# Kernel optimization log

Measured on AMD Instinct MI355X. Metric: run time of the kernel, lower is better.

The kernel has to match this reference:

```python
import jax, jax.numpy as jnp
import numpy as np

B, A, D, F, O, NB = 64, 1024, 5, 256, 256, 6  # batch, max_atoms, max_degree, ishape, oshape, bond feat dim


def setup_inputs() -> dict:
    key = jax.random.key(0)
    k1, k2, k3, k4 = jax.random.split(key, 4)
    atoms = jax.random.normal(k1, (B, A, F), dtype=jnp.float32)
    bonds = jax.random.normal(k2, (B, A, D, NB), dtype=jnp.float32)
    # -1 marks missing neighbor (degree padding); valid indices in [0, A)
    edges = jax.random.randint(k3, (B, A, D), -1, A)
    # xavier-normal-ish init for the 6 degree-specific weights, stacked [6, F+NB, O]
    scale = (2.0 / (F + NB + O)) ** 0.5
    degW = jax.random.normal(k4, (6, F + NB, O), dtype=jnp.float32) * scale
    b = jnp.full((1, O), 0.01, dtype=jnp.float32)
    return {"atoms": atoms, "bonds": bonds, "edges": edges, "degW": degW, "b": b}


def reference(atoms, bonds, edges, degW, b):
    # atoms: [B, A, F]; bonds: [B, A, D, NB]; edges: [B, A, D] int (-1 = pad)
    degrees = (edges != -1).sum(-1, keepdims=True)  # [B, A, 1]
    # pad a zero row at index 0 so edge -1 -> 0 gathers the mask value 0
    padded = jnp.pad(atoms, ((0, 0), (1, 0), (0, 0)))  # [B, A+1, F]
    neigh = jax.vmap(lambda p, e: p[e])(padded, edges + 1)  # [B, A, D, F]
    summed_atom = atoms + neigh.sum(axis=2)  # include_self=True
    feats = jnp.concatenate([summed_atom, bonds.sum(axis=2)], axis=-1)  # [B, A, F+NB]
    out = jnp.zeros((atoms.shape[0], atoms.shape[1], degW.shape[-1]), atoms.dtype)
    for d in range(6):  # fixed small structural loop over degree buckets
        mask = (degrees == d).astype(atoms.dtype)  # [B, A, 1]
        out = out + jax.nn.sigmoid(feats @ degW[d] + b) * mask
    return out
```

## Files before the change

### kernel.cpp

```cpp
#include <hip/hip_runtime.h>
#include <cstdint>

#define BATCH  64
#define NATOMS 1024
#define DEG    5
#define FIN    256
#define OOUT   256
#define NBF    6
#define KDIM   262
#define KP     288
#define MROWS  (BATCH * NATOMS)

typedef __attribute__((ext_vector_type(8))) short bf16x8;
typedef __attribute__((ext_vector_type(4))) float f32x4;

__device__ __forceinline__ unsigned short f2bf(float x) {
    unsigned u = __float_as_uint(x);
    u += 0x7fff + ((u >> 16) & 1);
    return (unsigned short)(u >> 16);
}
__device__ __forceinline__ float bf2f(unsigned short h) {
    return __uint_as_float(((unsigned)h) << 16);
}
__device__ __forceinline__ float sigmoidf_(float x) {
    return 1.f / (1.f + __expf(-x));
}

__global__ __launch_bounds__(256)
void convert_w_kernel(const float* __restrict__ degW, unsigned short* __restrict__ Wt)
{
    const int idx = blockIdx.x * 256 + threadIdx.x;
    if (idx >= 6 * KP * OOUT) return;
    const int d   = idx / (KP * OOUT);
    const int rem = idx % (KP * OOUT);
    const int k   = rem / OOUT;
    const int o   = rem % OOUT;
    const float v = (k < KDIM) ? degW[(size_t)d * KDIM * OOUT + (size_t)k * OOUT + o] : 0.f;
    Wt[(size_t)d * OOUT * KP + (size_t)o * KP + k] = f2bf(v);
}

__global__ __launch_bounds__(256)
void gather_kernel(const float* __restrict__ atoms, const float* __restrict__ bonds,
                   const int* __restrict__ edges, unsigned short* __restrict__ feats,
                   int* __restrict__ odd_list, int* __restrict__ odd_cnt)
{
    const int tid  = threadIdx.x;
    const int lane = tid & 63;
    const int w    = tid >> 6;
    const int row  = blockIdx.x * 4 + w;
    const int batch = row >> 10;

    const float4* arow = (const float4*)(atoms + (size_t)row * FIN);
    float4 v = arow[lane];
    int deg = 0;
    #pragma unroll
    for (int d = 0; d < DEG; ++d) {
        const int e = edges[row * DEG + d];
        if (e >= 0) {
            ++deg;
            const float4* nrow = (const float4*)(atoms + ((size_t)(batch << 10) + e) * FIN);
            const float4 nv = nrow[lane];
            v.x += nv.x; v.y += nv.y; v.z += nv.z; v.w += nv.w;
        }
    }
    ushort4 us;
    us.x = f2bf(v.x); us.y = f2bf(v.y); us.z = f2bf(v.z); us.w = f2bf(v.w);
    *(ushort4*)&feats[(size_t)row * KP + lane * 4] = us;

    if (lane < 32) {
        float bv = 0.f;
        if (lane < NBF) {
            const float* bb = bonds + (size_t)row * (DEG * NBF);
            #pragma unroll
            for (int d = 0; d < DEG; ++d) bv += bb[d * NBF + lane];
        }
        feats[(size_t)row * KP + FIN + lane] = f2bf(bv);
    }
    if (lane == 0 && deg != DEG) {
        const int i = atomicAdd(odd_cnt, 1);
        odd_list[i] = (row << 3) | deg;
    }
}

__global__ __launch_bounds__(256, 2)
void gemm_kernel(const unsigned short* __restrict__ feats,
                 const unsigned short* __restrict__ Wt5,
                 const float* __restrict__ bias, float* __restrict__ out)
{
    __shared__ short As[128 * 40];
    __shared__ short Bs[128 * 40];

    const int tid  = threadIdx.x;
    const int m0   = (blockIdx.x >> 1) * 128;
    const int n0   = (blockIdx.x & 1) * 128;
    const int lane = tid & 63;
    const int wave = tid >> 6;
    const int wm   = (wave & 1) * 64;
    const int wn   = (wave >> 1) * 64;
    const int fr   = lane & 15;
    const int q    = lane >> 4;

    f32x4 acc[4][4];
    #pragma unroll
    for (int i = 0; i < 4; ++i)
        #pragma unroll
        for (int j = 0; j < 4; ++j)
            acc[i][j] = (f32x4){0.f, 0.f, 0.f, 0.f};

    const unsigned short* Ag = feats + (size_t)m0 * KP;
    const unsigned short* Bg = Wt5  + (size_t)n0 * KP;

    for (int kt = 0; kt < KP; kt += 32) {
        __syncthreads();
        #pragma unroll
        for (int p = 0; p < 2; ++p) {
            const int idx = p * 256 + tid;
            const int r = idx >> 2, c = (idx & 3) * 8;
            *(uint4*)&As[r * 40 + c] = *(const uint4*)&Ag[(size_t)r * KP + kt + c];
            *(uint4*)&Bs[r * 40 + c] = *(const uint4*)&Bg[(size_t)r * KP + kt + c];
        }
        __syncthreads();

        bf16x8 af[4], bf[4];
        #pragma unroll
        for (int i = 0; i < 4; ++i)
            af[i] = *(const bf16x8*)&As[(wm + i * 16 + fr) * 40 + q * 8];
        #pragma unroll
        for (int j = 0; j < 4; ++j)
            bf[j] = *(const bf16x8*)&Bs[(wn + j * 16 + fr) * 40 + q * 8];
        #pragma unroll
        for (int i = 0; i < 4; ++i)
            #pragma unroll
            for (int j = 0; j < 4; ++j)
                acc[i][j] = __builtin_amdgcn_mfma_f32_16x16x32_bf16(af[i], bf[j], acc[i][j], 0, 0, 0);
    }

    #pragma unroll
    for (int j = 0; j < 4; ++j) {
        const int gn = n0 + wn + j * 16 + fr;
        const float bj = bias[gn];
        #pragma unroll
        for (int i = 0; i < 4; ++i) {
            #pragma unroll
            for (int r = 0; r < 4; ++r) {
                const int gm = m0 + wm + i * 16 + q * 4 + r;
                out[(size_t)gm * OOUT + gn] = sigmoidf_(acc[i][j][r] + bj);
            }
        }
    }
}

__global__ __launch_bounds__(256)
void fixup_kernel(const unsigned short* __restrict__ feats, const float* __restrict__ degW,
                  const float* __restrict__ bias, const int* __restrict__ odd_list,
                  const int* __restrict__ odd_cnt, float* __restrict__ out)
{
    const int cnt = *odd_cnt;
    const int tid = threadIdx.x;
    for (int i = blockIdx.x; i < cnt; i += gridDim.x) {
        const int packed = odd_list[i];
        const int row = packed >> 3;
        const int d   = packed & 7;
        const float* __restrict__ W = degW + (size_t)d * KDIM * OOUT;
        float acc = 0.f;
        for (int k = 0; k < KDIM; ++k)
            acc += bf2f(feats[(size_t)row * KP + k]) * W[(size_t)k * OOUT + tid];
        out[(size_t)row * OOUT + tid] = sigmoidf_(acc + bias[tid]);
    }
}

#define MT  32
#define KT  32
#define KPAD 288
__global__ __launch_bounds__(256, 2)
void nfp_conv_fallback(const float* __restrict__ atoms, const float* __restrict__ bonds,
                       const int* __restrict__ edges, const float* __restrict__ degW,
                       const float* __restrict__ bias, float* __restrict__ out)
{
    __shared__ float feats[MT * KPAD];
    __shared__ float wtile[KT * OOUT];
    __shared__ int   edg[MT * DEG];
    __shared__ int   deg_lds[MT];
    __shared__ int   odd_list[MT];
    __shared__ int   odd_cnt;
    __shared__ float b_lds[OOUT];

    const int tid = threadIdx.x, bid = blockIdx.x;
    const int batch = bid >> 5, a0 = (bid & 31) * MT;
    const size_t atom_base = (size_t)batch * NATOMS;

    b_lds[tid] = bias[tid];
    if (tid == 0) odd_cnt = 0;
    if (tid < MT * DEG) {
        const int m = tid / DEG, d = tid % DEG;
        edg[tid] = edges[(atom_base + a0 + m) * DEG + d];
    }
    __syncthreads();
    if (tid < MT) {
        int dc = 0;
        #pragma unroll
        for (int d = 0; d < DEG; ++d) dc += (edg[tid * DEG + d] != -1) ? 1 : 0;
        deg_lds[tid] = dc;
        if (dc != DEG) { const int idx = atomicAdd(&odd_cnt, 1); odd_list[idx] = tid; }
    }
    __syncthreads();
    {
        const int f = tid;
        for (int m = 0; m < MT; ++m) {
            float v = atoms[(atom_base + a0 + m) * FIN + f];
            #pragma unroll
            for (int d = 0; d < DEG; ++d) {
                const int e = edg[m * DEG + d];
                if (e >= 0) v += atoms[(atom_base + e) * FIN + f];
            }
            feats[m * KPAD + f] = v;
        }
        #pragma unroll
        for (int t = 0; t < 4; ++t) {
            const int idx = t * 256 + tid;
            const int m = idx >> 5, kk = idx & 31;
            float v = 0.f;
            if (kk < NBF) {
                const size_t bb = (atom_base + a0 + m) * (size_t)(DEG * NBF);
                #pragma unroll
                for (int d = 0; d < DEG; ++d) v += bonds[bb + d * NBF + kk];
            }
            feats[m * KPAD + FIN + kk] = v;
        }
    }
    const float* __restrict__ W5 = degW + (size_t)DEG * KDIM * OOUT;
    float acc[4][8];
    #pragma unroll
    for (int i = 0; i < 4; ++i)
        #pragma unroll
        for (int j = 0; j < 8; ++j) acc[i][j] = 0.f;
    const int tx = tid & 31, ty = tid >> 5;
    for (int kt = 0; kt < KPAD; kt += KT) {
        __syncthreads();
        #pragma unroll
        for (int t = 0; t < KT; ++t) {
            const int k = kt + t;
            wtile[t * OOUT + tid] = (k < KDIM) ? W5[(size_t)k * OOUT + tid] : 0.f;
        }
        __syncthreads();
        #pragma unroll 4
        for (int r = 0; r < KT; ++r) {
            float a_frag[4];
            #pragma unroll
            for (int i = 0; i < 4; ++i) a_frag[i] = feats[(ty * 4 + i) * KPAD + kt + r];
            float w_frag[8];
            #pragma unroll
            for (int j = 0; j < 8; ++j) w_frag[j] = wtile[r * OOUT + tx + j * 32];
            #pragma unroll
            for (int i = 0; i < 4; ++i)
                #pragma unroll
                for (int j = 0; j < 8; ++j) acc[i][j] += a_frag[i] * w_frag[j];
        }
    }
    #pragma unroll
    for (int i = 0; i < 4; ++i) {
        const int m = ty * 4 + i;
        if (deg_lds[m] == DEG) {
            const size_t row = (atom_base + a0 + m) * (size_t)OOUT;
            #pragma unroll
            for (int j = 0; j < 8; ++j) {
                const int o = tx + j * 32;
                out[row + o] = sigmoidf_(acc[i][j] + b_lds[o]);
            }
        }
    }
    const int ocnt = odd_cnt;
    for (int i = 0; i < ocnt; ++i) {
        const int m = odd_list[i], d = deg_lds[m];
        const float* __restrict__ W = degW + (size_t)d * KDIM * OOUT;
        float a2 = 0.f;
        for (int k = 0; k < KDIM; ++k) a2 += feats[m * KPAD + k] * W[(size_t)k * OOUT + tid];
        const size_t row = (atom_base + a0 + m) * (size_t)OOUT;
        out[row + tid] = sigmoidf_(a2 + b_lds[tid]);
    }
}

extern "C" void kernel_launch(void* const* d_in, const int* in_sizes, int n_in,
                              void* d_out, int out_size, void* d_ws, size_t ws_size,
                              hipStream_t stream) {
    const float* atoms = (const float*)d_in[0];
    const float* bonds = (const float*)d_in[1];
    const int*   edges = (const int*)d_in[2];
    const float* degW  = (const float*)d_in[3];
    const float* bias  = (const float*)d_in[4];
    float* out = (float*)d_out;

    const size_t FEATS_BYTES = (size_t)MROWS * KP * 2;
    const size_t WT_OFF      = FEATS_BYTES;
    const size_t WT_BYTES    = (size_t)6 * OOUT * KP * 2;
    const size_t ODD_OFF     = WT_OFF + WT_BYTES;
    const size_t ODD_BYTES   = (size_t)MROWS * 4;
    const size_t CNT_OFF     = ODD_OFF + ODD_BYTES;
    const size_t NEEDED      = CNT_OFF + 16;

    if (ws_size < NEEDED) {
        nfp_conv_fallback<<<BATCH * (NATOMS / MT), 256, 0, stream>>>(
            atoms, bonds, edges, degW, bias, out);
        return;
    }

    unsigned short* feats = (unsigned short*)d_ws;
    unsigned short* Wt    = (unsigned short*)((char*)d_ws + WT_OFF);
    int* odd_list         = (int*)((char*)d_ws + ODD_OFF);
    int* odd_cnt          = (int*)((char*)d_ws + CNT_OFF);

    hipMemsetAsync(odd_cnt, 0, 4, stream);
    convert_w_kernel<<<(6 * KP * OOUT) / 256, 256, 0, stream>>>(degW, Wt);
    gather_kernel<<<MROWS / 4, 256, 0, stream>>>(atoms, bonds, edges, feats, odd_list, odd_cnt);
    gemm_kernel<<<(MROWS / 128) * 2, 256, 0, stream>>>(
        feats, Wt + (size_t)5 * OOUT * KP, bias, out);
    fixup_kernel<<<512, 256, 0, stream>>>(feats, degW, bias, odd_list, odd_cnt, out);
}
```

Measured before the change: 222.1 us.

## Fuse gather, GEMM and odd-degree fixup into one kernel with pre-swizzled weights

Merges the neighbour gather, the degree-5 MFMA GEMM and the odd-degree fixup into one kernel. Each block builds a 64-row bf16 feature tile in LDS and reads weight fragments straight from global memory in a layout pre-swizzled to match MFMA operands. This removes the global feats round trip, the memset, the atomic odd list and two launches. Blocks are also mapped so each XCD handles whole batches, for L2 locality on neighbour gathers. The cost is that odd-degree rows are handled serially per block with scalar FMA loops, and weights are no longer staged in LDS.

```diff
diff --git a/kernel.cpp b/kernel.cpp
--- a/kernel.cpp
+++ b/kernel.cpp
@@ -9,7 +9,10 @@
 #define NBF    6
 #define KDIM   262
 #define KP     288
+#define NKT    9
 #define MROWS  (BATCH * NATOMS)
+#define MT     64
+#define AS     296
 
 typedef __attribute__((ext_vector_type(8))) short bf16x8;
 typedef __attribute__((ext_vector_type(4))) float f32x4;
@@ -27,78 +30,84 @@
 }
 
 __global__ __launch_bounds__(256)
-void convert_w_kernel(const float* __restrict__ degW, unsigned short* __restrict__ Wt)
+void convert_w_kernel(const float* __restrict__ degW, unsigned short* __restrict__ Wsw)
 {
     const int idx = blockIdx.x * 256 + threadIdx.x;
-    if (idx >= 6 * KP * OOUT) return;
-    const int d   = idx / (KP * OOUT);
-    const int rem = idx % (KP * OOUT);
-    const int k   = rem / OOUT;
-    const int o   = rem % OOUT;
-    const float v = (k < KDIM) ? degW[(size_t)d * KDIM * OOUT + (size_t)k * OOUT + o] : 0.f;
-    Wt[(size_t)d * OOUT * KP + (size_t)o * KP + k] = f2bf(v);
-}
-
-__global__ __launch_bounds__(256)
-void gather_kernel(const float* __restrict__ atoms, const float* __restrict__ bonds,
-                   const int* __restrict__ edges, unsigned short* __restrict__ feats,
-                   int* __restrict__ odd_list, int* __restrict__ odd_cnt)
+    if (idx >= 16 * NKT * 64) return;
+    const int lane = idx & 63;
+    const int t    = (idx >> 6) % NKT;
+    const int g    = (idx >> 6) / NKT;
+    const int col  = g * 16 + (lane & 15);
+    const int k0   = t * 32 + (lane >> 4) * 8;
+    const float* __restrict__ W5 = degW + (size_t)DEG * KDIM * OOUT;
+    unsigned short* dst = Wsw + (size_t)idx * 8;
+    #pragma unroll
+    for (int j = 0; j < 8; ++j) {
+        const int k = k0 + j;
+        dst[j] = f2bf((k < KDIM) ? W5[(size_t)k * OOUT + col] : 0.f);
+    }
+}
+
+__global__ __launch_bounds__(256, 4)
+void nfp_fused_kernel(const float* __restrict__ atoms, const float* __restrict__ bonds,
+                      const int* __restrict__ edges, const unsigned short* __restrict__ Wsw,
+                      const float* __restrict__ degW, const float* __restrict__ bias,
+                      float* __restrict__ out)
 {
+    __shared__ short Afeat[MT * AS];
+    __shared__ int   edg[MT * DEG];
+    __shared__ int   deg_lds[MT];
+
     const int tid  = threadIdx.x;
     const int lane = tid & 63;
-    const int w    = tid >> 6;
-    const int row  = blockIdx.x * 4 + w;
-    const int batch = row >> 10;
-
-    const float4* arow = (const float4*)(atoms + (size_t)row * FIN);
-    float4 v = arow[lane];
-    int deg = 0;
-    #pragma unroll
-    for (int d = 0; d < DEG; ++d) {
-        const int e = edges[row * DEG + d];
-        if (e >= 0) {
-            ++deg;
-            const float4* nrow = (const float4*)(atoms + ((size_t)(batch << 10) + e) * FIN);
-            const float4 nv = nrow[lane];
-            v.x += nv.x; v.y += nv.y; v.z += nv.z; v.w += nv.w;
-        }
-    }
-    ushort4 us;
-    us.x = f2bf(v.x); us.y = f2bf(v.y); us.z = f2bf(v.z); us.w = f2bf(v.w);
-    *(ushort4*)&feats[(size_t)row * KP + lane * 4] = us;
-
-    if (lane < 32) {
-        float bv = 0.f;
-        if (lane < NBF) {
-            const float* bb = bonds + (size_t)row * (DEG * NBF);
-            #pragma unroll
-            for (int d = 0; d < DEG; ++d) bv += bb[d * NBF + lane];
-        }
-        feats[(size_t)row * KP + FIN + lane] = f2bf(bv);
-    }
-    if (lane == 0 && deg != DEG) {
-        const int i = atomicAdd(odd_cnt, 1);
-        odd_list[i] = (row << 3) | deg;
-    }
-}
-
-__global__ __launch_bounds__(256, 2)
-void gemm_kernel(const unsigned short* __restrict__ feats,
-                 const unsigned short* __restrict__ Wt5,
-                 const float* __restrict__ bias, float* __restrict__ out)
-{
-    __shared__ short As[128 * 40];
-    __shared__ short Bs[128 * 40];
-
-    const int tid  = threadIdx.x;
-    const int m0   = (blockIdx.x >> 1) * 128;
-    const int n0   = (blockIdx.x & 1) * 128;
-    const int lane = tid & 63;
     const int wave = tid >> 6;
-    const int wm   = (wave & 1) * 64;
-    const int wn   = (wave >> 1) * 64;
-    const int fr   = lane & 15;
-    const int q    = lane >> 4;
+
+    const int bid   = blockIdx.x;
+    const int xcd   = bid & 7;
+    const int per   = bid >> 3;
+    const int batch = (per >> 4) * 8 + xcd;
+    const int blk   = per & 15;
+    const int row0  = batch * NATOMS + blk * MT;
+
+    for (int i = tid; i < MT * DEG; i += 256)
+        edg[i] = edges[row0 * DEG + i];
+    __syncthreads();
+    if (tid < MT) {
+        int dc = 0;
+        #pragma unroll
+        for (int d = 0; d < DEG; ++d) dc += (edg[tid * DEG + d] != -1) ? 1 : 0;
+        deg_lds[tid] = dc;
+    }
+
+    for (int mi = 0; mi < 16; ++mi) {
+        const int m = wave * 16 + mi;
+        float4 v = *(const float4*)&atoms[((size_t)row0 + m) * FIN + lane * 4];
+        #pragma unroll
+        for (int d = 0; d < DEG; ++d) {
+            const int e = edg[m * DEG + d];
+            if (e >= 0) {
+                const float4 nv = *(const float4*)&atoms[((size_t)(batch << 10) + e) * FIN + lane * 4];
+                v.x += nv.x; v.y += nv.y; v.z += nv.z; v.w += nv.w;
+            }
+        }
+        ushort4 us;
+        us.x = f2bf(v.x); us.y = f2bf(v.y); us.z = f2bf(v.z); us.w = f2bf(v.w);
+        *(ushort4*)&Afeat[m * AS + lane * 4] = us;
+        if (lane < 32) {
+            float bv = 0.f;
+            if (lane < NBF) {
+                const float* bb = bonds + ((size_t)row0 + m) * (DEG * NBF);
+                #pragma unroll
+                for (int d = 0; d < DEG; ++d) bv += bb[d * NBF + lane];
+            }
+            Afeat[m * AS + FIN + lane] = f2bf(bv);
+        }
+    }
+    __syncthreads();
+
+    const int fr = lane & 15;
+    const int q  = lane >> 4;
+    const int wn = wave * 64;
 
     f32x4 acc[4][4];
     #pragma unroll
@@ -107,96 +116,77 @@
         for (int j = 0; j < 4; ++j)
             acc[i][j] = (f32x4){0.f, 0.f, 0.f, 0.f};
 
-    const unsigned short* Ag = feats + (size_t)m0 * KP;
-    const unsigned short* Bg = Wt5  + (size_t)n0 * KP;
-
-    for (int kt = 0; kt < KP; kt += 32) {
-        __syncthreads();
-        #pragma unroll
-        for (int p = 0; p < 2; ++p) {
-            const int idx = p * 256 + tid;
-            const int r = idx >> 2, c = (idx & 3) * 8;
-            *(uint4*)&As[r * 40 + c] = *(const uint4*)&Ag[(size_t)r * KP + kt + c];
-            *(uint4*)&Bs[r * 40 + c] = *(const uint4*)&Bg[(size_t)r * KP + kt + c];
-        }
-        __syncthreads();
-
-        bf16x8 af[4], bf[4];
+    #pragma unroll
+    for (int t = 0; t < NKT; ++t) {
+        bf16x8 af[4], bfr[4];
         #pragma unroll
         for (int i = 0; i < 4; ++i)
-            af[i] = *(const bf16x8*)&As[(wm + i * 16 + fr) * 40 + q * 8];
+            af[i] = *(const bf16x8*)&Afeat[(i * 16 + fr) * AS + t * 32 + q * 8];
         #pragma unroll
         for (int j = 0; j < 4; ++j)
-            bf[j] = *(const bf16x8*)&Bs[(wn + j * 16 + fr) * 40 + q * 8];
+            bfr[j] = *(const bf16x8*)&Wsw[((size_t)((wave * 4 + j) * NKT + t) * 64 + lane) * 8];
         #pragma unroll
         for (int i = 0; i < 4; ++i)
             #pragma unroll
             for (int j = 0; j < 4; ++j)
-                acc[i][j] = __builtin_amdgcn_mfma_f32_16x16x32_bf16(af[i], bf[j], acc[i][j], 0, 0, 0);
+                acc[i][j] = __builtin_amdgcn_mfma_f32_16x16x32_bf16(af[i], bfr[j], acc[i][j], 0, 0, 0);
     }
 
     #pragma unroll
     for (int j = 0; j < 4; ++j) {
-        const int gn = n0 + wn + j * 16 + fr;
+        const int gn = wn + j * 16 + fr;
         const float bj = bias[gn];
         #pragma unroll
         for (int i = 0; i < 4; ++i) {
             #pragma unroll
             for (int r = 0; r < 4; ++r) {
-                const int gm = m0 + wm + i * 16 + q * 4 + r;
-                out[(size_t)gm * OOUT + gn] = sigmoidf_(acc[i][j][r] + bj);
-            }
-        }
-    }
-}
-
-__global__ __launch_bounds__(256)
-void fixup_kernel(const unsigned short* __restrict__ feats, const float* __restrict__ degW,
-                  const float* __restrict__ bias, const int* __restrict__ odd_list,
-                  const int* __restrict__ odd_cnt, float* __restrict__ out)
-{
-    const int cnt = *odd_cnt;
-    const int tid = threadIdx.x;
-    for (int i = blockIdx.x; i < cnt; i += gridDim.x) {
-        const int packed = odd_list[i];
-        const int row = packed >> 3;
-        const int d   = packed & 7;
+                const int lm = i * 16 + q * 4 + r;
+                if (deg_lds[lm] == DEG)
+                    out[((size_t)row0 + lm) * OOUT + gn] = sigmoidf_(acc[i][j][r] + bj);
+            }
+        }
+    }
+
+    for (int m = 0; m < MT; ++m) {
+        const int d = deg_lds[m];
+        if (d == DEG) continue;
         const float* __restrict__ W = degW + (size_t)d * KDIM * OOUT;
-        float acc = 0.f;
+        float a2 = 0.f;
+        #pragma unroll 2
         for (int k = 0; k < KDIM; ++k)
-            acc += bf2f(feats[(size_t)row * KP + k]) * W[(size_t)k * OOUT + tid];
-        out[(size_t)row * OOUT + tid] = sigmoidf_(acc + bias[tid]);
-    }
-}
-
-#define MT  32
-#define KT  32
-#define KPAD 288
+            a2 += bf2f(Afeat[m * AS + k]) * W[(size_t)k * OOUT + tid];
+        out[((size_t)row0 + m) * OOUT + tid] = sigmoidf_(a2 + bias[tid]);
+    }
+}
+
+#define FMT  32
+#define FKT  32
+#define FKPAD 288
 __global__ __launch_bounds__(256, 2)
 void nfp_conv_fallback(const float* __restrict__ atoms, const float* __restrict__ bonds,
                        const int* __restrict__ edges, const float* __restrict__ degW,
                        const float* __restrict__ bias, float* __restrict__ out)
 {
-    __shared__ float feats[MT * KPAD];
-    __shared__ float wtile[KT * OOUT];
-    __shared__ int   edg[MT * DEG];
-    __shared__ int   deg_lds[MT];
-    __shared__ int   odd_list[MT];
+    __shared__ float feats[FMT * FKPAD];
+    __shared__ float wtile[FKT * OOUT];
+    __shared__ int   edg[FMT * DEG];
+    __shared__ int   deg_lds[FMT];
+    __shared__ int   odd_list[FMT];
     __shared__ int   odd_cnt;
     __shared__ float b_lds[OOUT];
 
     const int tid = threadIdx.x, bid = blockIdx.x;
-    const int batch = bid >> 5, a0 = (bid & 31) * MT;
+    const int batch = bid >> 5, a0 = (bid & 31) * FMT;
     const size_t atom_base = (size_t)batch * NATOMS;
 
     b_lds[tid] = bias[tid];
     if (tid == 0) odd_cnt = 0;
-    if (tid < MT * DEG) {
+    if (tid < FMT * DEG) {
         const int m = tid / DEG, d = tid % DEG;
         edg[tid] = edges[(atom_base + a0 + m) * DEG + d];
     }
     __syncthreads();
-    if (tid < MT) {
+    if (tid < FMT) {
         int dc = 0;
         #pragma unroll
         for (int d = 0; d < DEG; ++d) dc += (edg[tid * DEG + d] != -1) ? 1 : 0;
@@ -206,14 +196,14 @@
     __syncthreads();
     {
         const int f = tid;
-        for (int m = 0; m < MT; ++m) {
+        for (int m = 0; m < FMT; ++m) {
             float v = atoms[(atom_base + a0 + m) * FIN + f];
             #pragma unroll
             for (int d = 0; d < DEG; ++d) {
                 const int e = edg[m * DEG + d];
                 if (e >= 0) v += atoms[(atom_base + e) * FIN + f];
             }
-            feats[m * KPAD + f] = v;
+            feats[m * FKPAD + f] = v;
         }
         #pragma unroll
         for (int t = 0; t < 4; ++t) {
@@ -225,7 +215,7 @@
                 #pragma unroll
                 for (int d = 0; d < DEG; ++d) v += bonds[bb + d * NBF + kk];
             }
-            feats[m * KPAD + FIN + kk] = v;
+            feats[m * FKPAD + FIN + kk] = v;
         }
     }
     const float* __restrict__ W5 = degW + (size_t)DEG * KDIM * OOUT;
@@ -235,19 +225,19 @@
         #pragma unroll
         for (int j = 0; j < 8; ++j) acc[i][j] = 0.f;
     const int tx = tid & 31, ty = tid >> 5;
-    for (int kt = 0; kt < KPAD; kt += KT) {
+    for (int kt = 0; kt < FKPAD; kt += FKT) {
         __syncthreads();
         #pragma unroll
-        for (int t = 0; t < KT; ++t) {
+        for (int t = 0; t < FKT; ++t) {
             const int k = kt + t;
             wtile[t * OOUT + tid] = (k < KDIM) ? W5[(size_t)k * OOUT + tid] : 0.f;
         }
         __syncthreads();
         #pragma unroll 4
-        for (int r = 0; r < KT; ++r) {
+        for (int r = 0; r < FKT; ++r) {
             float a_frag[4];
             #pragma unroll
-            for (int i = 0; i < 4; ++i) a_frag[i] = feats[(ty * 4 + i) * KPAD + kt + r];
+            for (int i = 0; i < 4; ++i) a_frag[i] = feats[(ty * 4 + i) * FKPAD + kt + r];
             float w_frag[8];
             #pragma unroll
             for (int j = 0; j < 8; ++j) w_frag[j] = wtile[r * OOUT + tx + j * 32];
@@ -274,7 +264,7 @@
         const int m = odd_list[i], d = deg_lds[m];
         const float* __restrict__ W = degW + (size_t)d * KDIM * OOUT;
         float a2 = 0.f;
-        for (int k = 0; k < KDIM; ++k) a2 += feats[m * KPAD + k] * W[(size_t)k * OOUT + tid];
+        for (int k = 0; k < KDIM; ++k) a2 += feats[m * FKPAD + k] * W[(size_t)k * OOUT + tid];
         const size_t row = (atom_base + a0 + m) * (size_t)OOUT;
         out[row + tid] = sigmoidf_(a2 + b_lds[tid]);
     }
@@ -290,29 +280,16 @@
     const float* bias  = (const float*)d_in[4];
     float* out = (float*)d_out;
 
-    const size_t FEATS_BYTES = (size_t)MROWS * KP * 2;
-    const size_t WT_OFF      = FEATS_BYTES;
-    const size_t WT_BYTES    = (size_t)6 * OOUT * KP * 2;
-    const size_t ODD_OFF     = WT_OFF + WT_BYTES;
-    const size_t ODD_BYTES   = (size_t)MROWS * 4;
-    const size_t CNT_OFF     = ODD_OFF + ODD_BYTES;
-    const size_t NEEDED      = CNT_OFF + 16;
-
-    if (ws_size < NEEDED) {
-        nfp_conv_fallback<<<BATCH * (NATOMS / MT), 256, 0, stream>>>(
+    const size_t WSW_BYTES = (size_t)16 * NKT * 64 * 8 * 2;
+
+    if (ws_size < WSW_BYTES) {
+        nfp_conv_fallback<<<BATCH * (NATOMS / FMT), 256, 0, stream>>>(
             atoms, bonds, edges, degW, bias, out);
         return;
     }
 
-    unsigned short* feats = (unsigned short*)d_ws;
-    unsigned short* Wt    = (unsigned short*)((char*)d_ws + WT_OFF);
-    int* odd_list         = (int*)((char*)d_ws + ODD_OFF);
-    int* odd_cnt          = (int*)((char*)d_ws + CNT_OFF);
-
-    hipMemsetAsync(odd_cnt, 0, 4, stream);
-    convert_w_kernel<<<(6 * KP * OOUT) / 256, 256, 0, stream>>>(degW, Wt);
-    gather_kernel<<<MROWS / 4, 256, 0, stream>>>(atoms, bonds, edges, feats, odd_list, odd_cnt);
-    gemm_kernel<<<(MROWS / 128) * 2, 256, 0, stream>>>(
-        feats, Wt + (size_t)5 * OOUT * KP, bias, out);
-    fixup_kernel<<<512, 256, 0, stream>>>(feats, degW, bias, odd_list, odd_cnt, out);
-}
+    unsigned short* Wsw = (unsigned short*)d_ws;
+    convert_w_kernel<<<(16 * NKT * 64 + 255) / 256, 256, 0, stream>>>(degW, Wsw);
+    nfp_fused_kernel<<<MROWS / MT, 256, 0, stream>>>(
+        atoms, bonds, edges, Wsw, degW, bias, out);
+}
```

New measurement: 255.5 us. 1.15x slower.
